# Optimization experiments

Measured on AMD Instinct MI355X. Metric: run time of the kernel, lower is better.

Reference implementation:

```python
import jax, jax.numpy as jnp
import numpy as np

V, H, T = 32000, 1024, 512


def setup_inputs() -> dict:
    key = jax.random.key(0)
    ks = jax.random.split(key, 5)
    tokens = jax.random.randint(ks[0], (T, 1), 0, V)  # sequence of batch-1 token ids
    E = jax.random.normal(ks[1], (V, H), dtype=jnp.float32) * 0.02   # embedding Linear weight^T
    b_e = jnp.zeros((H,), dtype=jnp.float32)
    # stacked gate weights [4, 2H, H] for (input, output, forget, cell) gates
    W_r = jax.random.normal(ks[2], (4, 2 * H, H), dtype=jnp.float32) * 0.02
    b_r = jnp.zeros((4, H), dtype=jnp.float32)
    W_l = jax.random.normal(ks[3], (4, 2 * H, H), dtype=jnp.float32) * 0.02
    b_l = jnp.zeros((4, H), dtype=jnp.float32)
    return {"tokens": tokens, "E": E, "b_e": b_e, "W_r": W_r, "b_r": b_r, "W_l": W_l, "b_l": b_l}


def _lstm_scan(emb_seq, W, b):
    """emb_seq: [T, 1, H]; W: [4, 2H, H]; b: [4, H]. Returns (all hiddens [T,1,H], h, c)."""
    def step(carry, x):
        h, c = carry
        comb = jnp.concatenate([x, h], axis=1)                      # [1, 2H]
        gates = jnp.einsum('bi,gio->gbo', comb, W) + b[:, None, :]  # [4, 1, H]
        i_g = jax.nn.sigmoid(gates[0])
        o_g = jax.nn.sigmoid(gates[1])
        f_g = jax.nn.sigmoid(gates[2])
        c_g = jnp.tanh(gates[3])
        c = f_g * c + i_g * c_g
        h = o_g * jnp.tanh(c)
        return (h, c), h
    init = (jnp.zeros((1, H), emb_seq.dtype), jnp.zeros((1, H), emb_seq.dtype))
    (h, c), hs = jax.lax.scan(step, init, emb_seq)
    return hs, h, c


def reference(tokens, E, b_e, W_r, b_r, W_l, b_l):
    # one_hot(tok, V) @ Linear(V,H) == row gather from E plus bias
    emb = E[tokens] + b_e                      # [T, 1, H]
    hs_f, h_f, c_f = _lstm_scan(emb, W_r, b_r)         # forward direction
    hs_b, _, _ = _lstm_scan(emb[::-1], W_l, b_l)       # backward direction
    # NOTE: faithful to source bug/behavior: backward states are concatenated in
    # reverse-iteration order (not flipped back before concat).
    annotations = jnp.concatenate([hs_f, hs_b], axis=-1)  # [T, 1, 2H]
    return annotations, h_f, c_f
```

## Files before the change

kernel.cpp:

```cpp
#include <hip/hip_runtime.h>

#define TT 512
#define HH 1024
#define NC 8192
#define TAGBASE 0x40000000u

#define WS_GX    0
#define WS_EMB   4194304
#define WS_X     4194304

__device__ __forceinline__ float rdlane(float v, int l) {
  return __int_as_float(__builtin_amdgcn_readlane(__float_as_int(v), l));
}
__device__ __forceinline__ float fsig(float x) {
  float e = __builtin_amdgcn_exp2f(-1.44269504f * x);
  return __builtin_amdgcn_rcpf(1.f + e);
}
__device__ __forceinline__ float ftanh(float x) {
  float e = __builtin_amdgcn_exp2f(2.88539009f * x);
  return fmaf(-2.f, __builtin_amdgcn_rcpf(1.f + e), 1.f);
}

__global__ __launch_bounds__(256) void k_embed(const int* __restrict__ tok,
                                               const float* __restrict__ E,
                                               const float* __restrict__ be,
                                               float* __restrict__ emb) {
  int i = blockIdx.x * 256 + threadIdx.x;
  int t = i >> 10, h = i & (HH - 1);
  emb[i] = E[(size_t)tok[t] * HH + h] + be[h];
}

__global__ __launch_bounds__(256) void k_gemm(const float* __restrict__ emb,
                                              const float* __restrict__ Wr,
                                              const float* __restrict__ Wl,
                                              const float* __restrict__ br,
                                              const float* __restrict__ bl,
                                              float* __restrict__ Gx) {
  __shared__ float As[32][132];
  __shared__ float Bs[32][68];
  int ct = blockIdx.x, ttile = blockIdx.y;
  int tid = threadIdx.x;
  int d = ct >> 6;
  int bp = ct & 63;
  int u0 = bp << 4;
  const float* W = d ? Wl : Wr;
  const float* bias = d ? bl : br;
  int t0 = ttile * 128;
  int tc = tid & 15, tr = tid >> 4;

  float acc[8][4];
#pragma unroll
  for (int i = 0; i < 8; ++i)
#pragma unroll
    for (int j = 0; j < 4; ++j) acc[i][j] = 0.f;

  int sk = tid & 31, st = tid >> 5;
  int sc = tid & 63, skb = tid >> 6;
  int sg = sc & 3, su = u0 + (sc >> 2);

  for (int k0 = 0; k0 < HH; k0 += 32) {
    __syncthreads();
#pragma unroll
    for (int pass = 0; pass < 16; ++pass) {
      int t = st + (pass << 3);
      As[sk][t] = emb[(size_t)(t0 + t) * HH + k0 + sk];
    }
#pragma unroll
    for (int pass = 0; pass < 8; ++pass) {
      int k = skb + (pass << 2);
      Bs[k][sc] = W[((size_t)sg * 2048 + k0 + k) * HH + su];
    }
    __syncthreads();
#pragma unroll
    for (int k = 0; k < 32; ++k) {
      float4 bv = *(const float4*)&Bs[k][tc << 2];
      float4 a0 = *(const float4*)&As[k][tr << 3];
      float4 a1 = *(const float4*)&As[k][(tr << 3) + 4];
      float av[8] = {a0.x, a0.y, a0.z, a0.w, a1.x, a1.y, a1.z, a1.w};
#pragma unroll
      for (int i = 0; i < 8; ++i) {
        acc[i][0] = fmaf(av[i], bv.x, acc[i][0]);
        acc[i][1] = fmaf(av[i], bv.y, acc[i][1]);
        acc[i][2] = fmaf(av[i], bv.z, acc[i][2]);
        acc[i][3] = fmaf(av[i], bv.w, acc[i][3]);
      }
    }
  }
  int c0 = ct << 6;
  float b0 = bias[0 * HH + u0 + tc];
  float b1 = bias[1 * HH + u0 + tc];
  float b2 = bias[2 * HH + u0 + tc];
  float b3 = bias[3 * HH + u0 + tc];
#pragma unroll
  for (int i = 0; i < 8; ++i) {
    int t = t0 + (tr << 3) + i;
    float4 o;
    o.x = acc[i][0] + b0;
    o.y = acc[i][1] + b1;
    o.z = acc[i][2] + b2;
    o.w = acc[i][3] + b3;
    *(float4*)&Gx[(size_t)t * NC + c0 + (tc << 2)] = o;
  }
}

__global__ __launch_bounds__(1024, 1) void k_scan(const float* __restrict__ Wr,
                                                  const float* __restrict__ Wl,
                                                  const float* __restrict__ Gx,
                                                  unsigned long long* __restrict__ xch,
                                                  float* __restrict__ out) {
  int b = blockIdx.x;
  int d = b >> 6, bp = b & 63;
  int tid = threadIdx.x;
  int w = tid >> 6, l = tid & 63;
  int u0 = bp << 4;
  int g = l & 3, ur = l >> 2;
  const float* W = d ? Wl : Wr;

  float wreg[64];
  {
    const float* wb = W + ((size_t)g * 2048 + HH + (w << 6)) * HH + (u0 + ur);
#pragma unroll
    for (int j = 0; j < 64; ++j) wreg[j] = wb[(size_t)j * HH];
  }

  __shared__ float red[2][16][64];
  float c_reg = 0.f;
  const float* gxbase = Gx + (d << 12) + (bp << 6);
  unsigned long long* xd = xch + ((size_t)d << 10);

  for (int t = 0; t < TT; ++t) {
    int p = t & 1;
    float s_gx = 0.f;
    if (w == 0) {
      int rt = d ? (TT - 1 - t) : t;
      s_gx = gxbase[(size_t)rt * NC + l];
    }

    float partial = 0.f;
    if (t > 0) {
      unsigned long long* slot = xd + (((size_t)(t - 1)) << 11) + (w << 6) + l;
      unsigned int want = TAGBASE + (unsigned int)t;
      unsigned long long v;
      while (true) {
        v = __hip_atomic_load(slot, __ATOMIC_RELAXED, __HIP_MEMORY_SCOPE_AGENT);
        if (__all((unsigned int)(v >> 32) == want)) break;
        __builtin_amdgcn_s_sleep(1);
      }
      float hv = __int_as_float((int)(unsigned int)v);
      float acc0 = 0.f, acc1 = 0.f;
#pragma unroll
      for (int j = 0; j < 64; j += 2) {
        acc0 = fmaf(rdlane(hv, j), wreg[j], acc0);
        acc1 = fmaf(rdlane(hv, j + 1), wreg[j + 1], acc1);
      }
      partial = acc0 + acc1;
    }
    red[p][w][l] = partial;
    __syncthreads();

    if (w == 0) {
      float sval = s_gx;
#pragma unroll
      for (int ww = 0; ww < 16; ++ww) sval += red[p][ww][l];
      int lb = l & ~3;
      float gi = __shfl(sval, lb + 0);
      float go = __shfl(sval, lb + 1);
      float gf = __shfl(sval, lb + 2);
      float gc = __shfl(sval, lb + 3);
      float ig = fsig(gi);
      float og = fsig(go);
      float fg = fsig(gf);
      float cg = ftanh(gc);
      c_reg = fg * c_reg + ig * cg;
      float hval = og * ftanh(c_reg);

      if (g == 0) {
        int uu = u0 + ur;
        unsigned long long val =
            (((unsigned long long)(TAGBASE + (unsigned int)(t + 1))) << 32) |
            (unsigned int)__float_as_int(hval);
        __hip_atomic_store(xd + (((size_t)t) << 11) + uu, val, __ATOMIC_RELAXED,
                           __HIP_MEMORY_SCOPE_AGENT);
        out[(size_t)t * 2048 + (d << 10) + uu] = hval;
        if (d == 0 && t == TT - 1) {
          out[(size_t)TT * 2048 + uu] = hval;
          out[(size_t)TT * 2048 + HH + uu] = c_reg;
        }
      }
    }
  }
}

extern "C" void kernel_launch(void* const* d_in, const int* in_sizes, int n_in,
                              void* d_out, int out_size, void* d_ws, size_t ws_size,
                              hipStream_t stream) {
  const int* tok = (const int*)d_in[0];
  const float* E = (const float*)d_in[1];
  const float* be = (const float*)d_in[2];
  const float* Wr = (const float*)d_in[3];
  const float* br = (const float*)d_in[4];
  const float* Wl = (const float*)d_in[5];
  const float* bl = (const float*)d_in[6];
  float* out = (float*)d_out;
  float* ws = (float*)d_ws;

  float* Gx = ws + WS_GX;
  float* emb = ws + WS_EMB;
  unsigned long long* xch = (unsigned long long*)(ws + WS_X);


  k_embed<<<dim3(TT * HH / 256), dim3(256), 0, stream>>>(tok, E, be, emb);
  k_gemm<<<dim3(128, 4), dim3(256), 0, stream>>>(emb, Wr, Wl, br, bl, Gx);
  k_scan<<<dim3(128), dim3(1024), 0, stream>>>(Wr, Wl, Gx, xch, out);
}
```

Baseline: 1.277 ms.

## Fuse embedding gather into input GEMM and switch to gate-major column layout

Result: no change. 1.284 ms (+0.5%).

```diff
diff --git a/kernel.cpp b/kernel.cpp
--- a/kernel.cpp
+++ b/kernel.cpp
@@ -6,7 +6,6 @@
 #define TAGBASE 0x40000000u
 
 #define WS_GX    0
-#define WS_EMB   4194304
 #define WS_X     4194304
 
 __device__ __forceinline__ float rdlane(float v, int l) {
@@ -21,16 +20,9 @@
   return fmaf(-2.f, __builtin_amdgcn_rcpf(1.f + e), 1.f);
 }
 
-__global__ __launch_bounds__(256) void k_embed(const int* __restrict__ tok,
-                                               const float* __restrict__ E,
-                                               const float* __restrict__ be,
-                                               float* __restrict__ emb) {
-  int i = blockIdx.x * 256 + threadIdx.x;
-  int t = i >> 10, h = i & (HH - 1);
-  emb[i] = E[(size_t)tok[t] * HH + h] + be[h];
-}
-
-__global__ __launch_bounds__(256) void k_gemm(const float* __restrict__ emb,
+__global__ __launch_bounds__(256) void k_gemm(const int* __restrict__ tok,
+                                              const float* __restrict__ E,
+                                              const float* __restrict__ be,
                                               const float* __restrict__ Wr,
                                               const float* __restrict__ Wl,
                                               const float* __restrict__ br,
@@ -38,6 +30,7 @@
                                               float* __restrict__ Gx) {
   __shared__ float As[32][132];
   __shared__ float Bs[32][68];
+  __shared__ int tokL[128];
   int ct = blockIdx.x, ttile = blockIdx.y;
   int tid = threadIdx.x;
   int d = ct >> 6;
@@ -48,27 +41,37 @@
   int t0 = ttile * 128;
   int tc = tid & 15, tr = tid >> 4;
 
+  if (tid < 128) tokL[tid] = tok[t0 + tid];
+
   float acc[8][4];
 #pragma unroll
   for (int i = 0; i < 8; ++i)
 #pragma unroll
     for (int j = 0; j < 4; ++j) acc[i][j] = 0.f;
 
-  int sk = tid & 31, st = tid >> 5;
-  int sc = tid & 63, skb = tid >> 6;
-  int sg = sc & 3, su = u0 + (sc >> 2);
+  int a_tl = tid >> 3, a_kq = (tid & 7) << 2;
+  int b_k = tid >> 4, b_c0 = (tid & 15) << 2;
+  int b_g = b_c0 >> 4;
+  int b_u = u0 + (b_c0 & 15);
 
   for (int k0 = 0; k0 < HH; k0 += 32) {
     __syncthreads();
 #pragma unroll
-    for (int pass = 0; pass < 16; ++pass) {
-      int t = st + (pass << 3);
-      As[sk][t] = emb[(size_t)(t0 + t) * HH + k0 + sk];
-    }
-#pragma unroll
-    for (int pass = 0; pass < 8; ++pass) {
-      int k = skb + (pass << 2);
-      Bs[k][sc] = W[((size_t)sg * 2048 + k0 + k) * HH + su];
+    for (int p = 0; p < 4; ++p) {
+      int tl = a_tl + (p << 5);
+      int row = tokL[tl];
+      float4 ev = *(const float4*)&E[(size_t)row * HH + k0 + a_kq];
+      float4 bv4 = *(const float4*)&be[k0 + a_kq];
+      As[a_kq + 0][tl] = ev.x + bv4.x;
+      As[a_kq + 1][tl] = ev.y + bv4.y;
+      As[a_kq + 2][tl] = ev.z + bv4.z;
+      As[a_kq + 3][tl] = ev.w + bv4.w;
+    }
+#pragma unroll
+    for (int p = 0; p < 2; ++p) {
+      int k = b_k + (p << 4);
+      float4 wv = *(const float4*)&W[((size_t)b_g * 2048 + k0 + k) * HH + b_u];
+      *(float4*)&Bs[k][b_c0] = wv;
     }
     __syncthreads();
 #pragma unroll
@@ -86,11 +89,13 @@
       }
     }
   }
-  int c0 = ct << 6;
-  float b0 = bias[0 * HH + u0 + tc];
-  float b1 = bias[1 * HH + u0 + tc];
-  float b2 = bias[2 * HH + u0 + tc];
-  float b3 = bias[3 * HH + u0 + tc];
+  int cg = tc >> 2;
+  int cu = u0 + ((tc & 3) << 2);
+  float b0 = bias[cg * HH + cu + 0];
+  float b1 = bias[cg * HH + cu + 1];
+  float b2 = bias[cg * HH + cu + 2];
+  float b3 = bias[cg * HH + cu + 3];
+  size_t cbase = (size_t)(d << 12) + (bp << 6) + (tc << 2);
 #pragma unroll
   for (int i = 0; i < 8; ++i) {
     int t = t0 + (tr << 3) + i;
@@ -99,7 +104,7 @@
     o.y = acc[i][1] + b1;
     o.z = acc[i][2] + b2;
     o.w = acc[i][3] + b3;
-    *(float4*)&Gx[(size_t)t * NC + c0 + (tc << 2)] = o;
+    *(float4*)&Gx[(size_t)t * NC + cbase] = o;
   }
 }
 
@@ -113,7 +118,7 @@
   int tid = threadIdx.x;
   int w = tid >> 6, l = tid & 63;
   int u0 = bp << 4;
-  int g = l & 3, ur = l >> 2;
+  int g = l >> 4, ur = l & 15;
   const float* W = d ? Wl : Wr;
 
   float wreg[64];
@@ -162,20 +167,20 @@
       float sval = s_gx;
 #pragma unroll
       for (int ww = 0; ww < 16; ++ww) sval += red[p][ww][l];
-      int lb = l & ~3;
-      float gi = __shfl(sval, lb + 0);
-      float go = __shfl(sval, lb + 1);
-      float gf = __shfl(sval, lb + 2);
-      float gc = __shfl(sval, lb + 3);
+      int uu4 = l & 15;
+      float gi = __shfl(sval, uu4);
+      float go = __shfl(sval, 16 + uu4);
+      float gf = __shfl(sval, 32 + uu4);
+      float gc = __shfl(sval, 48 + uu4);
       float ig = fsig(gi);
       float og = fsig(go);
       float fg = fsig(gf);
-      float cg = ftanh(gc);
-      c_reg = fg * c_reg + ig * cg;
+      float cg2 = ftanh(gc);
+      c_reg = fg * c_reg + ig * cg2;
       float hval = og * ftanh(c_reg);
 
-      if (g == 0) {
-        int uu = u0 + ur;
+      if (l < 16) {
+        int uu = u0 + l;
         unsigned long long val =
             (((unsigned long long)(TAGBASE + (unsigned int)(t + 1))) << 32) |
             (unsigned int)__float_as_int(hval);
@@ -205,11 +210,9 @@
   float* ws = (float*)d_ws;
 
   float* Gx = ws + WS_GX;
-  float* emb = ws + WS_EMB;
   unsigned long long* xch = (unsigned long long*)(ws + WS_X);
 
 
-  k_embed<<<dim3(TT * HH / 256), dim3(256), 0, stream>>>(tok, E, be, emb);
-  k_gemm<<<dim3(128, 4), dim3(256), 0, stream>>>(emb, Wr, Wl, br, bl, Gx);
+  k_gemm<<<dim3(128, 4), dim3(256), 0, stream>>>(tok, E, be, Wr, Wl, br, bl, Gx);
   k_scan<<<dim3(128), dim3(1024), 0, stream>>>(Wr, Wl, Gx, xch, out);
 }
```
